# Kernel optimization log

Measured on AMD Instinct MI355X. Metric: run time of the kernel, lower is better.

## Reference

```python
import jax, jax.numpy as jnp
import numpy as np

D_IN = 512
D = 1024      # new_embed_dim
H = 16        # num_heads
HD = D // H   # head_dim


def setup_inputs() -> dict:
    key = jax.random.key(0)
    ks = jax.random.split(key, 16)
    g = lambda k, shape, fan: jax.random.normal(k, shape, jnp.float32) / np.sqrt(fan)
    return {
        "x1": jax.random.normal(ks[0], (16, 1, D_IN), jnp.float32),
        "x2": jax.random.normal(ks[1], (16, 4096, D_IN), jnp.float32),
        "x3": jax.random.normal(ks[2], (16, 4096, D_IN), jnp.float32),
        # embedding1 (for x1) and embedding2 (used for BOTH x2 and x3, per source)
        "We1": g(ks[3], (D_IN, D), D_IN), "be1": jnp.zeros((D,), jnp.float32),
        "We2": g(ks[4], (D_IN, D), D_IN), "be2": jnp.zeros((D,), jnp.float32),
        "Wq": g(ks[5], (D, D), D), "bq": jnp.zeros((D,), jnp.float32),
        "Wk": g(ks[6], (D, D), D), "bk": jnp.zeros((D,), jnp.float32),
        "Wv": g(ks[7], (D, D), D), "bv": jnp.zeros((D,), jnp.float32),
        "Wo": g(ks[8], (D, D), D), "bo": jnp.zeros((D,), jnp.float32),
    }


def reference(x1, x2, x3, We1, be1, We2, be2, Wq, bq, Wk, bk, Wv, bv, Wo, bo):
    B = x1.shape[0]
    # embeddings (x3 intentionally uses embedding2's weights, matching source)
    x1e = x1 @ We1 + be1                      # [B,1,D]
    x2e = x2 @ We2 + be2                      # [B,S,D]
    x3e = x3 @ We2 + be2                      # [B,S,D]
    q = (x1e @ Wq + bq).reshape(B, -1, H, HD).transpose(0, 2, 1, 3)  # [B,H,1,HD]
    k = (x2e @ Wk + bk).reshape(B, -1, H, HD).transpose(0, 2, 1, 3)  # [B,H,S,HD]
    v = (x3e @ Wv + bv).reshape(B, -1, H, HD).transpose(0, 2, 1, 3)  # [B,H,S,HD]
    scale = jnp.asarray(np.sqrt(HD), q.dtype)
    attn = jax.nn.softmax(jnp.einsum("bhqd,bhkd->bhqk", q, k) / scale, axis=-1)
    # dropout is identity at inference (keras training=False default)
    av = jnp.einsum("bhqk,bhkd->bhqd", attn, v)          # [B,H,1,HD]
    av = av.transpose(0, 2, 1, 3).reshape(B, -1, D)      # [B,1,D]
    out = av @ Wo + bo                                   # [B,1,D]
    return jnp.squeeze(out, axis=1)                      # [B,D]
```

## Files before the change

kernel.cpp:

```cpp
#include <hip/hip_runtime.h>


#define DIN 512
#define DD  1024
#define NH  16
#define HD  64
#define BB  16
#define SS  4096
#define NCH 64

__device__ __forceinline__ int wave_id() {
    return __builtin_amdgcn_readfirstlane((int)(threadIdx.x >> 6));
}

__device__ __forceinline__ void tile_transpose(const float* __restrict__ in,
                                               float* __restrict__ out,
                                               int R, int C, int rblk, int cblk) {
    __shared__ float tl[32][33];
    const int tx = threadIdx.x & 31, ty = threadIdx.x >> 5;
    const int c0 = cblk * 32, r0 = rblk * 32;
#pragma unroll
    for (int k = 0; k < 4; ++k)
        tl[ty + k * 8][tx] = in[(size_t)(r0 + ty + k * 8) * C + c0 + tx];
    __syncthreads();
#pragma unroll
    for (int k = 0; k < 4; ++k)
        out[(size_t)(c0 + ty + k * 8) * R + r0 + tx] = tl[tx][ty + k * 8];
}

__global__ __launch_bounds__(256) void k_prep(const float* __restrict__ We2,
                                              const float* __restrict__ Wk,
                                              const float* __restrict__ be1,
                                              const float* __restrict__ bq,
                                              const float* __restrict__ bv,
                                              const float* __restrict__ bo,
                                              float* __restrict__ We2t,
                                              float* __restrict__ WkT,
                                              float* __restrict__ x1e,
                                              float* __restrict__ qb,
                                              float* __restrict__ av,
                                              float* __restrict__ out) {
    const int bx = blockIdx.x;
    if (bx < 512) {
        tile_transpose(We2, We2t, DIN, DD, bx >> 5, bx & 31);
    } else if (bx < 1536) {
        const int lb = bx - 512;
        tile_transpose(Wk, WkT, DD, DD, lb >> 5, lb & 31);
    } else {
        const int b = bx - 1536;
#pragma unroll
        for (int k = 0; k < 4; ++k) {
            const int c = k * 256 + threadIdx.x;
            x1e[(size_t)b * DD + c] = be1[c];
            qb[(size_t)b * DD + c]  = bq[c];
            av[(size_t)b * DD + c]  = bv[c];
            out[(size_t)b * DD + c] = bo[c];
        }
    }
}

template <int K, int N, int KS, bool HASB>
__global__ __launch_bounds__(256) void k_bmv2(const float* __restrict__ in,
                                              const float* __restrict__ W,
                                              const float* __restrict__ bias,
                                              float* __restrict__ out) {
    const int l = threadIdx.x & 63;
    const int c = blockIdx.x * 64 + l;
    const int wv = wave_id();
    constexpr int KCH = K / KS;
    constexpr int SUB = KCH / 4;
    const float* inb = in + (size_t)blockIdx.y * 16 * K;
    float acc[16];
#pragma unroll
    for (int r = 0; r < 16; ++r) acc[r] = 0.f;
    const int i0 = blockIdx.z * KCH + wv * SUB;
#pragma unroll 4
    for (int i = i0; i < i0 + SUB; ++i) {
        const float wval = W[(size_t)i * N + c];
#pragma unroll
        for (int r = 0; r < 16; ++r) acc[r] += inb[(size_t)r * K + i] * wval;
    }
    __shared__ float red[4][16][64];
#pragma unroll
    for (int r = 0; r < 16; ++r) red[wv][r][l] = acc[r];
    __syncthreads();
#pragma unroll
    for (int k = 0; k < 4; ++k) {
        const int r = wv + k * 4;
        float v = red[0][r][l] + red[1][r][l] + red[2][r][l] + red[3][r][l];
        float* dst = out + ((size_t)blockIdx.y * 16 + r) * N + c;
        if (KS == 1) {
            if (HASB) v += bias[c];
            *dst = v;
        } else {
            atomicAdd(dst, v);
        }
    }
}

__global__ __launch_bounds__(256) void k_u2(const float* __restrict__ q,
                                            const float* __restrict__ WkT,
                                            float* __restrict__ u) {
    const int h = blockIdx.y;
    const int l = threadIdx.x & 63;
    const int c = blockIdx.x * 64 + l;
    const int wv = wave_id();
    float acc[16];
#pragma unroll
    for (int bb = 0; bb < 16; ++bb) acc[bb] = 0.f;
#pragma unroll 4
    for (int dk = 0; dk < 16; ++dk) {
        const int d = wv * 16 + dk;
        const float wval = WkT[(size_t)(h * HD + d) * DD + c];
#pragma unroll
        for (int bb = 0; bb < 16; ++bb)
            acc[bb] += q[(size_t)bb * DD + h * HD + d] * wval;
    }
    __shared__ float red[4][16][64];
#pragma unroll
    for (int bb = 0; bb < 16; ++bb) red[wv][bb][l] = acc[bb];
    __syncthreads();
#pragma unroll
    for (int k = 0; k < 4; ++k) {
        const int bb = wv + k * 4;
        float v = red[0][bb][l] + red[1][bb][l] + red[2][bb][l] + red[3][bb][l];
        u[((size_t)bb * NH + h) * DD + c] = v;
    }
}

__global__ __launch_bounds__(512, 8) void k_attn(const float* __restrict__ x2,
                                                 const float* __restrict__ x3,
                                                 const float* __restrict__ w,
                                                 float* __restrict__ gp,
                                                 float* __restrict__ mls) {
    __shared__ __align__(16) float4 tile[64 * 33];
    __shared__ __align__(16) float etab[64 * 20];

    const int b = blockIdx.y, ch = blockIdx.x;
    const int l = threadIdx.x & 63;
    const int wv = wave_id();
    const int h0 = wv * 2;
    const int s0 = ch * 64;
    const float4* wp = (const float4*)(w + ((size_t)b * NH + h0) * DIN);
    const float4* x2f = (const float4*)x2 + ((size_t)b * SS + s0) * (DIN / 4);

    const int srow = threadIdx.x >> 5;
    const int sc4  = threadIdx.x & 31;
    float4 r0 = x2f[(size_t)(srow)      * 128 + sc4];
    float4 r1 = x2f[(size_t)(srow + 16) * 128 + sc4];
    float4 r2 = x2f[(size_t)(srow + 32) * 128 + sc4];
    float4 r3 = x2f[(size_t)(srow + 48) * 128 + sc4];
    float a0 = 0.f, a1 = 0.f;
    for (int kt = 0; kt < 4; ++kt) {
        __syncthreads();
        tile[(srow)      * 33 + sc4] = r0;
        tile[(srow + 16) * 33 + sc4] = r1;
        tile[(srow + 32) * 33 + sc4] = r2;
        tile[(srow + 48) * 33 + sc4] = r3;
        __syncthreads();
        if (kt < 3) {
            const int kc = (kt + 1) * 32 + sc4;
            r0 = x2f[(size_t)(srow)      * 128 + kc];
            r1 = x2f[(size_t)(srow + 16) * 128 + kc];
            r2 = x2f[(size_t)(srow + 32) * 128 + kc];
            r3 = x2f[(size_t)(srow + 48) * 128 + kc];
        }
#pragma unroll 8
        for (int c4 = 0; c4 < 32; ++c4) {
            const float4 x = tile[l * 33 + c4];
            const float4 q0 = wp[kt * 32 + c4];
            const float4 q1 = wp[128 + kt * 32 + c4];
            a0 += x.x * q0.x + x.y * q0.y + x.z * q0.z + x.w * q0.w;
            a1 += x.x * q1.x + x.y * q1.y + x.z * q1.z + x.w * q1.w;
        }
    }

    const float sc0 = a0 * 0.125f, sc1 = a1 * 0.125f;
    float m0 = sc0, m1 = sc1;
#pragma unroll
    for (int off = 1; off < 64; off <<= 1) {
        m0 = fmaxf(m0, __shfl_xor(m0, off));
        m1 = fmaxf(m1, __shfl_xor(m1, off));
    }
    const float e0 = __expf(sc0 - m0), e1 = __expf(sc1 - m1);
    etab[l * 20 + h0]     = e0;
    etab[l * 20 + h0 + 1] = e1;
    float ls0 = e0, ls1 = e1;
#pragma unroll
    for (int off = 1; off < 64; off <<= 1) {
        ls0 += __shfl_xor(ls0, off);
        ls1 += __shfl_xor(ls1, off);
    }
    if (l == 0) {
        float* dst = mls + (((size_t)b * NCH + ch) * NH + h0) * 2;
        dst[0] = m0; dst[1] = ls0;
        dst[2] = m1; dst[3] = ls1;
    }
    __syncthreads();

    const int colh = wv & 1;
    const int h4 = (wv >> 1) * 4;
    const float4* x3f = (const float4*)(x3 + ((size_t)b * SS + s0) * DIN)
                        + colh * 64 + l;
    float4 A0 = make_float4(0.f, 0.f, 0.f, 0.f);
    float4 A1 = make_float4(0.f, 0.f, 0.f, 0.f);
    float4 A2 = make_float4(0.f, 0.f, 0.f, 0.f);
    float4 A3 = make_float4(0.f, 0.f, 0.f, 0.f);

    float4 p0 = x3f[0 * 128], p1 = x3f[1 * 128];
    float4 p2 = x3f[2 * 128], p3 = x3f[3 * 128];
#pragma unroll 4
    for (int j = 0; j < 64; ++j) {
        const float4 xv = p0;
        p0 = p1; p1 = p2; p2 = p3;
        const int jn = (j + 4 < 64) ? (j + 4) : 63;
        p3 = x3f[(size_t)jn * 128];
        const float4 e4 = *(const float4*)&etab[j * 20 + h4];
        A0.x += e4.x * xv.x; A0.y += e4.x * xv.y; A0.z += e4.x * xv.z; A0.w += e4.x * xv.w;
        A1.x += e4.y * xv.x; A1.y += e4.y * xv.y; A1.z += e4.y * xv.z; A1.w += e4.y * xv.w;
        A2.x += e4.z * xv.x; A2.y += e4.z * xv.y; A2.z += e4.z * xv.z; A2.w += e4.z * xv.w;
        A3.x += e4.w * xv.x; A3.y += e4.w * xv.y; A3.z += e4.w * xv.z; A3.w += e4.w * xv.w;
    }

    float* gb = gp + ((size_t)(b * NCH + ch) * NH + h4) * DIN + colh * 256 + 4 * l;
    *(float4*)(gb + 0 * DIN) = A0;
    *(float4*)(gb + 1 * DIN) = A1;
    *(float4*)(gb + 2 * DIN) = A2;
    *(float4*)(gb + 3 * DIN) = A3;
}

__global__ __launch_bounds__(256) void k_greduce2(const float* __restrict__ gp,
                                                  const float* __restrict__ mls,
                                                  float* __restrict__ g) {
    const int bx = blockIdx.x;
    const int pair = bx >> 1;
    const int b = pair >> 4, h = pair & 15;
    const int i = (bx & 1) * 256 + threadIdx.x;
    const float* mbase = mls + ((size_t)b * NCH * NH + h) * 2;
    float M = -1e30f;
#pragma unroll 8
    for (int ch = 0; ch < NCH; ++ch)
        M = fmaxf(M, mbase[(size_t)ch * NH * 2]);
    float L = 0.f;
#pragma unroll 8
    for (int ch = 0; ch < NCH; ++ch)
        L += __expf(mbase[(size_t)ch * NH * 2] - M) * mbase[(size_t)ch * NH * 2 + 1];
    const float invL = 1.f / L;
    const float* gpb = gp + ((size_t)(b * NCH) * NH + h) * DIN + i;
    float acc = 0.f;
#pragma unroll 8
    for (int ch = 0; ch < NCH; ++ch)
        acc += __expf(mbase[(size_t)ch * NH * 2] - M) * gpb[(size_t)ch * NH * DIN];
    g[(size_t)pair * DIN + i] = acc * invL;
}

__global__ __launch_bounds__(256) void k_av_at(const float* __restrict__ G2,
                                               const float* __restrict__ Wv,
                                               float* __restrict__ av) {
    const int h = blockIdx.x;
    const int l = threadIdx.x & 63;
    const int wv = wave_id();
    const int c0 = blockIdx.y * 128 + wv * 32;
    float acc[16];
#pragma unroll
    for (int bb = 0; bb < 16; ++bb) acc[bb] = 0.f;
#pragma unroll 4
    for (int c = c0; c < c0 + 32; ++c) {
        const float wval = Wv[(size_t)c * DD + h * HD + l];
#pragma unroll
        for (int bb = 0; bb < 16; ++bb)
            acc[bb] += G2[((size_t)bb * NH + h) * DD + c] * wval;
    }
    __shared__ float red[4][16][64];
#pragma unroll
    for (int bb = 0; bb < 16; ++bb) red[wv][bb][l] = acc[bb];
    __syncthreads();
#pragma unroll
    for (int k = 0; k < 4; ++k) {
        const int bb = wv + k * 4;
        float v = red[0][bb][l] + red[1][bb][l] + red[2][bb][l] + red[3][bb][l];
        atomicAdd(&av[(size_t)bb * DD + h * HD + l], v);
    }
}

extern "C" void kernel_launch(void* const* d_in, const int* in_sizes, int n_in,
                              void* d_out, int out_size, void* d_ws, size_t ws_size,
                              hipStream_t stream) {
    const float* x1  = (const float*)d_in[0];
    const float* x2  = (const float*)d_in[1];
    const float* x3  = (const float*)d_in[2];
    const float* We1 = (const float*)d_in[3];
    const float* be1 = (const float*)d_in[4];
    const float* We2 = (const float*)d_in[5];
    const float* be2 = (const float*)d_in[6];
    const float* Wq  = (const float*)d_in[7];
    const float* bq  = (const float*)d_in[8];
    const float* Wk  = (const float*)d_in[9];
    const float* bk  = (const float*)d_in[10];
    const float* Wv  = (const float*)d_in[11];
    const float* bv  = (const float*)d_in[12];
    const float* Wo  = (const float*)d_in[13];
    const float* bo  = (const float*)d_in[14];
    (void)bk;
    float* out = (float*)d_out;

    char* ws = (char*)d_ws;
    size_t off = 0;
    auto alloc = [&](size_t bytes) -> void* {
        void* p = ws + off;
        off = (off + bytes + 255) & ~(size_t)255;
        return p;
    };
    float* We2t = (float*)alloc((size_t)DD * DIN * 4);
    float* WkT  = (float*)alloc((size_t)DD * DD * 4);
    float* x1e  = (float*)alloc((size_t)BB * DD * 4);
    float* qb   = (float*)alloc((size_t)BB * DD * 4);
    float* u    = (float*)alloc((size_t)BB * NH * DD * 4);
    float* wv_  = (float*)alloc((size_t)BB * NH * DIN * 4);
    float* g    = (float*)alloc((size_t)BB * NH * DIN * 4);
    float* G2   = (float*)alloc((size_t)BB * NH * DD * 4);
    float* av   = (float*)alloc((size_t)BB * DD * 4);
    float* gp   = (float*)alloc((size_t)BB * NCH * NH * DIN * 4);
    float* mls  = (float*)alloc((size_t)BB * NCH * NH * 2 * 4);

    k_prep<<<1552, 256, 0, stream>>>(We2, Wk, be1, bq, bv, bo,
                                     We2t, WkT, x1e, qb, av, out);
    k_bmv2<DIN, DD, 8, false><<<dim3(DD / 64, 1, 8), 256, 0, stream>>>(x1, We1, nullptr, x1e);
    k_bmv2<DD, DD, 8, false><<<dim3(DD / 64, 1, 8), 256, 0, stream>>>(x1e, Wq, nullptr, qb);
    k_u2<<<dim3(DD / 64, NH), 256, 0, stream>>>(qb, WkT, u);
    k_bmv2<DD, DIN, 1, false><<<dim3(DIN / 64, BB * NH / 16, 1), 256, 0, stream>>>(u, We2t, nullptr, wv_);
    k_attn<<<dim3(NCH, BB), 512, 0, stream>>>(x2, x3, wv_, gp, mls);
    k_greduce2<<<BB * NH * 2, 256, 0, stream>>>(gp, mls, g);
    k_bmv2<DIN, DD, 1, true><<<dim3(DD / 64, BB * NH / 16, 1), 256, 0, stream>>>(g, We2, be2, G2);
    k_av_at<<<dim3(NH, 8), 256, 0, stream>>>(G2, Wv, av);
    k_bmv2<DD, DD, 8, false><<<dim3(DD / 64, 1, 8), 256, 0, stream>>>(av, Wo, nullptr, out);
}
```

Measured before the change: 446.0 us.

## Rebalance attention scoring to 4 heads per wave with split-K LDS reduction

The attention kernel's score phase now gives each wave 4 heads over half of the input dimension, and the two halves are combined through shared memory, so each LDS tile load serves more heads. The tile and exp-table buffers are aliased to cut shared memory use, and the x3 prefetch is issued before the barrier. The group-reduce kernel is vectorised with float4 and uses fewer, narrower blocks, and several matvec loops are unrolled by 8. The change adds barriers and a reduction step, and only half the waves do the softmax work.

```diff
diff --git a/kernel.cpp b/kernel.cpp
--- a/kernel.cpp
+++ b/kernel.cpp
@@ -74,7 +74,7 @@
 #pragma unroll
     for (int r = 0; r < 16; ++r) acc[r] = 0.f;
     const int i0 = blockIdx.z * KCH + wv * SUB;
-#pragma unroll 4
+#pragma unroll 8
     for (int i = i0; i < i0 + SUB; ++i) {
         const float wval = W[(size_t)i * N + c];
 #pragma unroll
@@ -108,7 +108,7 @@
     float acc[16];
 #pragma unroll
     for (int bb = 0; bb < 16; ++bb) acc[bb] = 0.f;
-#pragma unroll 4
+#pragma unroll 8
     for (int dk = 0; dk < 16; ++dk) {
         const int d = wv * 16 + dk;
         const float wval = WkT[(size_t)(h * HD + d) * DD + c];
@@ -133,13 +133,18 @@
                                                  const float* __restrict__ w,
                                                  float* __restrict__ gp,
                                                  float* __restrict__ mls) {
-    __shared__ __align__(16) float4 tile[64 * 33];
-    __shared__ __align__(16) float etab[64 * 20];
+    __shared__ __align__(16) char smem[64 * 33 * 16];
+    float4* tile = (float4*)smem;
+    float*  scp  = (float*)smem;
+    float*  etab = (float*)(smem + 8192);
 
     const int b = blockIdx.y, ch = blockIdx.x;
     const int l = threadIdx.x & 63;
     const int wv = wave_id();
-    const int h0 = wv * 2;
+    const int hq  = wv & 3;
+    const int ch2 = wv >> 2;
+    const int h0 = hq * 4;
+    const int c4b = ch2 * 16;
     const int s0 = ch * 64;
     const float4* wp = (const float4*)(w + ((size_t)b * NH + h0) * DIN);
     const float4* x2f = (const float4*)x2 + ((size_t)b * SS + s0) * (DIN / 4);
@@ -150,7 +155,7 @@
     float4 r1 = x2f[(size_t)(srow + 16) * 128 + sc4];
     float4 r2 = x2f[(size_t)(srow + 32) * 128 + sc4];
     float4 r3 = x2f[(size_t)(srow + 48) * 128 + sc4];
-    float a0 = 0.f, a1 = 0.f;
+    float a0 = 0.f, a1 = 0.f, a2 = 0.f, a3 = 0.f;
     for (int kt = 0; kt < 4; ++kt) {
         __syncthreads();
         tile[(srow)      * 33 + sc4] = r0;
@@ -166,49 +171,75 @@
             r3 = x2f[(size_t)(srow + 48) * 128 + kc];
         }
 #pragma unroll 8
-        for (int c4 = 0; c4 < 32; ++c4) {
-            const float4 x = tile[l * 33 + c4];
-            const float4 q0 = wp[kt * 32 + c4];
-            const float4 q1 = wp[128 + kt * 32 + c4];
+        for (int k = 0; k < 16; ++k) {
+            const float4 x = tile[l * 33 + c4b + k];
+            const float4 q0 = wp[      kt * 32 + c4b + k];
+            const float4 q1 = wp[128 + kt * 32 + c4b + k];
+            const float4 q2 = wp[256 + kt * 32 + c4b + k];
+            const float4 q3 = wp[384 + kt * 32 + c4b + k];
             a0 += x.x * q0.x + x.y * q0.y + x.z * q0.z + x.w * q0.w;
             a1 += x.x * q1.x + x.y * q1.y + x.z * q1.z + x.w * q1.w;
-        }
-    }
-
-    const float sc0 = a0 * 0.125f, sc1 = a1 * 0.125f;
-    float m0 = sc0, m1 = sc1;
-#pragma unroll
-    for (int off = 1; off < 64; off <<= 1) {
-        m0 = fmaxf(m0, __shfl_xor(m0, off));
-        m1 = fmaxf(m1, __shfl_xor(m1, off));
-    }
-    const float e0 = __expf(sc0 - m0), e1 = __expf(sc1 - m1);
-    etab[l * 20 + h0]     = e0;
-    etab[l * 20 + h0 + 1] = e1;
-    float ls0 = e0, ls1 = e1;
-#pragma unroll
-    for (int off = 1; off < 64; off <<= 1) {
-        ls0 += __shfl_xor(ls0, off);
-        ls1 += __shfl_xor(ls1, off);
-    }
-    if (l == 0) {
-        float* dst = mls + (((size_t)b * NCH + ch) * NH + h0) * 2;
-        dst[0] = m0; dst[1] = ls0;
-        dst[2] = m1; dst[3] = ls1;
-    }
-    __syncthreads();
+            a2 += x.x * q2.x + x.y * q2.y + x.z * q2.z + x.w * q2.w;
+            a3 += x.x * q3.x + x.y * q3.y + x.z * q3.z + x.w * q3.w;
+        }
+    }
+
+    __syncthreads();
+    if (ch2 == 1) {
+        scp[(hq * 4 + 0) * 64 + l] = a0;
+        scp[(hq * 4 + 1) * 64 + l] = a1;
+        scp[(hq * 4 + 2) * 64 + l] = a2;
+        scp[(hq * 4 + 3) * 64 + l] = a3;
+    }
+    __syncthreads();
+
+    if (ch2 == 0) {
+        a0 += scp[(hq * 4 + 0) * 64 + l];
+        a1 += scp[(hq * 4 + 1) * 64 + l];
+        a2 += scp[(hq * 4 + 2) * 64 + l];
+        a3 += scp[(hq * 4 + 3) * 64 + l];
+        const float sc0 = a0 * 0.125f, sc1 = a1 * 0.125f;
+        const float sc2 = a2 * 0.125f, sc3 = a3 * 0.125f;
+        float m0 = sc0, m1 = sc1, m2 = sc2, m3 = sc3;
+#pragma unroll
+        for (int off = 1; off < 64; off <<= 1) {
+            m0 = fmaxf(m0, __shfl_xor(m0, off));
+            m1 = fmaxf(m1, __shfl_xor(m1, off));
+            m2 = fmaxf(m2, __shfl_xor(m2, off));
+            m3 = fmaxf(m3, __shfl_xor(m3, off));
+        }
+        const float e0 = __expf(sc0 - m0), e1 = __expf(sc1 - m1);
+        const float e2 = __expf(sc2 - m2), e3 = __expf(sc3 - m3);
+        *(float4*)&etab[l * 20 + h0] = make_float4(e0, e1, e2, e3);
+        float ls0 = e0, ls1 = e1, ls2 = e2, ls3 = e3;
+#pragma unroll
+        for (int off = 1; off < 64; off <<= 1) {
+            ls0 += __shfl_xor(ls0, off);
+            ls1 += __shfl_xor(ls1, off);
+            ls2 += __shfl_xor(ls2, off);
+            ls3 += __shfl_xor(ls3, off);
+        }
+        if (l == 0) {
+            float* dst = mls + (((size_t)b * NCH + ch) * NH + h0) * 2;
+            dst[0] = m0; dst[1] = ls0;
+            dst[2] = m1; dst[3] = ls1;
+            dst[4] = m2; dst[5] = ls2;
+            dst[6] = m3; dst[7] = ls3;
+        }
+    }
 
     const int colh = wv & 1;
     const int h4 = (wv >> 1) * 4;
     const float4* x3f = (const float4*)(x3 + ((size_t)b * SS + s0) * DIN)
                         + colh * 64 + l;
+    float4 p0 = x3f[0 * 128], p1 = x3f[1 * 128];
+    float4 p2 = x3f[2 * 128], p3 = x3f[3 * 128];
+    __syncthreads();
+
     float4 A0 = make_float4(0.f, 0.f, 0.f, 0.f);
     float4 A1 = make_float4(0.f, 0.f, 0.f, 0.f);
     float4 A2 = make_float4(0.f, 0.f, 0.f, 0.f);
     float4 A3 = make_float4(0.f, 0.f, 0.f, 0.f);
-
-    float4 p0 = x3f[0 * 128], p1 = x3f[1 * 128];
-    float4 p2 = x3f[2 * 128], p3 = x3f[3 * 128];
 #pragma unroll 4
     for (int j = 0; j < 64; ++j) {
         const float4 xv = p0;
@@ -229,13 +260,12 @@
     *(float4*)(gb + 3 * DIN) = A3;
 }
 
-__global__ __launch_bounds__(256) void k_greduce2(const float* __restrict__ gp,
+__global__ __launch_bounds__(128) void k_greduce2(const float* __restrict__ gp,
                                                   const float* __restrict__ mls,
                                                   float* __restrict__ g) {
-    const int bx = blockIdx.x;
-    const int pair = bx >> 1;
+    const int pair = blockIdx.x;
     const int b = pair >> 4, h = pair & 15;
-    const int i = (bx & 1) * 256 + threadIdx.x;
+    const int t = threadIdx.x;
     const float* mbase = mls + ((size_t)b * NCH * NH + h) * 2;
     float M = -1e30f;
 #pragma unroll 8
@@ -246,12 +276,16 @@
     for (int ch = 0; ch < NCH; ++ch)
         L += __expf(mbase[(size_t)ch * NH * 2] - M) * mbase[(size_t)ch * NH * 2 + 1];
     const float invL = 1.f / L;
-    const float* gpb = gp + ((size_t)(b * NCH) * NH + h) * DIN + i;
-    float acc = 0.f;
-#pragma unroll 8
-    for (int ch = 0; ch < NCH; ++ch)
-        acc += __expf(mbase[(size_t)ch * NH * 2] - M) * gpb[(size_t)ch * NH * DIN];
-    g[(size_t)pair * DIN + i] = acc * invL;
+    const float4* gpb = (const float4*)(gp + ((size_t)(b * NCH) * NH + h) * DIN) + t;
+    float4 acc = make_float4(0.f, 0.f, 0.f, 0.f);
+#pragma unroll 8
+    for (int ch = 0; ch < NCH; ++ch) {
+        const float f = __expf(mbase[(size_t)ch * NH * 2] - M);
+        const float4 v = gpb[(size_t)ch * NH * (DIN / 4)];
+        acc.x += f * v.x; acc.y += f * v.y; acc.z += f * v.z; acc.w += f * v.w;
+    }
+    acc.x *= invL; acc.y *= invL; acc.z *= invL; acc.w *= invL;
+    ((float4*)(g + (size_t)pair * DIN))[t] = acc;
 }
 
 __global__ __launch_bounds__(256) void k_av_at(const float* __restrict__ G2,
@@ -264,7 +298,7 @@
     float acc[16];
 #pragma unroll
     for (int bb = 0; bb < 16; ++bb) acc[bb] = 0.f;
-#pragma unroll 4
+#pragma unroll 8
     for (int c = c0; c < c0 + 32; ++c) {
         const float wval = Wv[(size_t)c * DD + h * HD + l];
 #pragma unroll
@@ -330,7 +364,7 @@
     k_u2<<<dim3(DD / 64, NH), 256, 0, stream>>>(qb, WkT, u);
     k_bmv2<DD, DIN, 1, false><<<dim3(DIN / 64, BB * NH / 16, 1), 256, 0, stream>>>(u, We2t, nullptr, wv_);
     k_attn<<<dim3(NCH, BB), 512, 0, stream>>>(x2, x3, wv_, gp, mls);
-    k_greduce2<<<BB * NH * 2, 256, 0, stream>>>(gp, mls, g);
+    k_greduce2<<<BB * NH, 128, 0, stream>>>(gp, mls, g);
     k_bmv2<DIN, DD, 1, true><<<dim3(DD / 64, BB * NH / 16, 1), 256, 0, stream>>>(g, We2, be2, G2);
     k_av_at<<<dim3(NH, 8), 256, 0, stream>>>(G2, Wv, av);
     k_bmv2<DD, DD, 8, false><<<dim3(DD / 64, 1, 8), 256, 0, stream>>>(av, Wo, nullptr, out);
```

Result: slower. 466.0 us (+4.5%).

## Double attention chunk size, use nontemporal streaming loads, vectorize partial reduce

Applied to the files above, without the earlier changes.

Each attention block now covers 128 sequence rows instead of 64, which halves the number of chunks and the partial-output traffic. x2, x3 and the partials are read with nontemporal loads. The first x3 prefetch is moved before the barrier, the softmax-partial reduce is vectorized with float4, and several small GEMV loops get a higher unroll factor. The price is half as many attention blocks (512) on a large GPU, which may lower latency hiding, plus higher register and LDS use per block.

```diff
diff --git a/kernel.cpp b/kernel.cpp
--- a/kernel.cpp
+++ b/kernel.cpp
@@ -7,7 +7,14 @@
 #define HD  64
 #define BB  16
 #define SS  4096
-#define NCH 64
+#define NCH 32
+
+typedef float vf4 __attribute__((ext_vector_type(4)));
+
+__device__ __forceinline__ float4 ldnt(const float4* p) {
+    vf4 v = __builtin_nontemporal_load((const vf4*)p);
+    return make_float4(v[0], v[1], v[2], v[3]);
+}
 
 __device__ __forceinline__ int wave_id() {
     return __builtin_amdgcn_readfirstlane((int)(threadIdx.x >> 6));
@@ -74,7 +81,7 @@
 #pragma unroll
     for (int r = 0; r < 16; ++r) acc[r] = 0.f;
     const int i0 = blockIdx.z * KCH + wv * SUB;
-#pragma unroll 4
+#pragma unroll 8
     for (int i = i0; i < i0 + SUB; ++i) {
         const float wval = W[(size_t)i * N + c];
 #pragma unroll
@@ -108,7 +115,7 @@
     float acc[16];
 #pragma unroll
     for (int bb = 0; bb < 16; ++bb) acc[bb] = 0.f;
-#pragma unroll 4
+#pragma unroll 8
     for (int dk = 0; dk < 16; ++dk) {
         const int d = wv * 16 + dk;
         const float wval = WkT[(size_t)(h * HD + d) * DD + c];
@@ -134,23 +141,49 @@
                                                  float* __restrict__ gp,
                                                  float* __restrict__ mls) {
     __shared__ __align__(16) float4 tile[64 * 33];
-    __shared__ __align__(16) float etab[64 * 20];
+    __shared__ __align__(16) float etab[128 * 20];
 
     const int b = blockIdx.y, ch = blockIdx.x;
     const int l = threadIdx.x & 63;
     const int wv = wave_id();
     const int h0 = wv * 2;
-    const int s0 = ch * 64;
+    const int s0 = ch * 128;
     const float4* wp = (const float4*)(w + ((size_t)b * NH + h0) * DIN);
     const float4* x2f = (const float4*)x2 + ((size_t)b * SS + s0) * (DIN / 4);
 
     const int srow = threadIdx.x >> 5;
     const int sc4  = threadIdx.x & 31;
-    float4 r0 = x2f[(size_t)(srow)      * 128 + sc4];
-    float4 r1 = x2f[(size_t)(srow + 16) * 128 + sc4];
-    float4 r2 = x2f[(size_t)(srow + 32) * 128 + sc4];
-    float4 r3 = x2f[(size_t)(srow + 48) * 128 + sc4];
-    float a0 = 0.f, a1 = 0.f;
+    float4 r0 = ldnt(&x2f[(size_t)(srow)      * 128 + sc4]);
+    float4 r1 = ldnt(&x2f[(size_t)(srow + 16) * 128 + sc4]);
+    float4 r2 = ldnt(&x2f[(size_t)(srow + 32) * 128 + sc4]);
+    float4 r3 = ldnt(&x2f[(size_t)(srow + 48) * 128 + sc4]);
+    float a00 = 0.f, a10 = 0.f;
+    float a01 = 0.f, a11 = 0.f;
+
+    for (int kt = 0; kt < 4; ++kt) {
+        __syncthreads();
+        tile[(srow)      * 33 + sc4] = r0;
+        tile[(srow + 16) * 33 + sc4] = r1;
+        tile[(srow + 32) * 33 + sc4] = r2;
+        tile[(srow + 48) * 33 + sc4] = r3;
+        __syncthreads();
+        {
+            const int rb = (kt < 3) ? 0 : 64;
+            const int kc = ((kt < 3) ? (kt + 1) : 0) * 32 + sc4;
+            r0 = ldnt(&x2f[(size_t)(rb + srow)      * 128 + kc]);
+            r1 = ldnt(&x2f[(size_t)(rb + srow + 16) * 128 + kc]);
+            r2 = ldnt(&x2f[(size_t)(rb + srow + 32) * 128 + kc]);
+            r3 = ldnt(&x2f[(size_t)(rb + srow + 48) * 128 + kc]);
+        }
+#pragma unroll 8
+        for (int c4 = 0; c4 < 32; ++c4) {
+            const float4 x = tile[l * 33 + c4];
+            const float4 q0 = wp[kt * 32 + c4];
+            const float4 q1 = wp[128 + kt * 32 + c4];
+            a00 += x.x * q0.x + x.y * q0.y + x.z * q0.z + x.w * q0.w;
+            a10 += x.x * q1.x + x.y * q1.y + x.z * q1.z + x.w * q1.w;
+        }
+    }
     for (int kt = 0; kt < 4; ++kt) {
         __syncthreads();
         tile[(srow)      * 33 + sc4] = r0;
@@ -160,32 +193,36 @@
         __syncthreads();
         if (kt < 3) {
             const int kc = (kt + 1) * 32 + sc4;
-            r0 = x2f[(size_t)(srow)      * 128 + kc];
-            r1 = x2f[(size_t)(srow + 16) * 128 + kc];
-            r2 = x2f[(size_t)(srow + 32) * 128 + kc];
-            r3 = x2f[(size_t)(srow + 48) * 128 + kc];
+            r0 = ldnt(&x2f[(size_t)(64 + srow)      * 128 + kc]);
+            r1 = ldnt(&x2f[(size_t)(64 + srow + 16) * 128 + kc]);
+            r2 = ldnt(&x2f[(size_t)(64 + srow + 32) * 128 + kc]);
+            r3 = ldnt(&x2f[(size_t)(64 + srow + 48) * 128 + kc]);
         }
 #pragma unroll 8
         for (int c4 = 0; c4 < 32; ++c4) {
             const float4 x = tile[l * 33 + c4];
             const float4 q0 = wp[kt * 32 + c4];
             const float4 q1 = wp[128 + kt * 32 + c4];
-            a0 += x.x * q0.x + x.y * q0.y + x.z * q0.z + x.w * q0.w;
-            a1 += x.x * q1.x + x.y * q1.y + x.z * q1.z + x.w * q1.w;
-        }
-    }
-
-    const float sc0 = a0 * 0.125f, sc1 = a1 * 0.125f;
-    float m0 = sc0, m1 = sc1;
+            a01 += x.x * q0.x + x.y * q0.y + x.z * q0.z + x.w * q0.w;
+            a11 += x.x * q1.x + x.y * q1.y + x.z * q1.z + x.w * q1.w;
+        }
+    }
+
+    const float sc00 = a00 * 0.125f, sc10 = a10 * 0.125f;
+    const float sc01 = a01 * 0.125f, sc11 = a11 * 0.125f;
+    float m0 = fmaxf(sc00, sc01), m1 = fmaxf(sc10, sc11);
 #pragma unroll
     for (int off = 1; off < 64; off <<= 1) {
         m0 = fmaxf(m0, __shfl_xor(m0, off));
         m1 = fmaxf(m1, __shfl_xor(m1, off));
     }
-    const float e0 = __expf(sc0 - m0), e1 = __expf(sc1 - m1);
-    etab[l * 20 + h0]     = e0;
-    etab[l * 20 + h0 + 1] = e1;
-    float ls0 = e0, ls1 = e1;
+    const float e00 = __expf(sc00 - m0), e01 = __expf(sc01 - m0);
+    const float e10 = __expf(sc10 - m1), e11 = __expf(sc11 - m1);
+    etab[l * 20 + h0]            = e00;
+    etab[l * 20 + h0 + 1]        = e10;
+    etab[(64 + l) * 20 + h0]     = e01;
+    etab[(64 + l) * 20 + h0 + 1] = e11;
+    float ls0 = e00 + e01, ls1 = e10 + e11;
 #pragma unroll
     for (int off = 1; off < 64; off <<= 1) {
         ls0 += __shfl_xor(ls0, off);
@@ -196,25 +233,25 @@
         dst[0] = m0; dst[1] = ls0;
         dst[2] = m1; dst[3] = ls1;
     }
-    __syncthreads();
 
     const int colh = wv & 1;
     const int h4 = (wv >> 1) * 4;
     const float4* x3f = (const float4*)(x3 + ((size_t)b * SS + s0) * DIN)
                         + colh * 64 + l;
+    float4 p0 = ldnt(&x3f[0 * 128]), p1 = ldnt(&x3f[1 * 128]);
+    float4 p2 = ldnt(&x3f[2 * 128]), p3 = ldnt(&x3f[3 * 128]);
+    __syncthreads();
+
     float4 A0 = make_float4(0.f, 0.f, 0.f, 0.f);
     float4 A1 = make_float4(0.f, 0.f, 0.f, 0.f);
     float4 A2 = make_float4(0.f, 0.f, 0.f, 0.f);
     float4 A3 = make_float4(0.f, 0.f, 0.f, 0.f);
-
-    float4 p0 = x3f[0 * 128], p1 = x3f[1 * 128];
-    float4 p2 = x3f[2 * 128], p3 = x3f[3 * 128];
 #pragma unroll 4
-    for (int j = 0; j < 64; ++j) {
+    for (int j = 0; j < 128; ++j) {
         const float4 xv = p0;
         p0 = p1; p1 = p2; p2 = p3;
-        const int jn = (j + 4 < 64) ? (j + 4) : 63;
-        p3 = x3f[(size_t)jn * 128];
+        const int jn = (j + 4 < 128) ? (j + 4) : 127;
+        p3 = ldnt(&x3f[(size_t)jn * 128]);
         const float4 e4 = *(const float4*)&etab[j * 20 + h4];
         A0.x += e4.x * xv.x; A0.y += e4.x * xv.y; A0.z += e4.x * xv.z; A0.w += e4.x * xv.w;
         A1.x += e4.y * xv.x; A1.y += e4.y * xv.y; A1.z += e4.y * xv.z; A1.w += e4.y * xv.w;
@@ -229,13 +266,12 @@
     *(float4*)(gb + 3 * DIN) = A3;
 }
 
-__global__ __launch_bounds__(256) void k_greduce2(const float* __restrict__ gp,
+__global__ __launch_bounds__(128) void k_greduce2(const float* __restrict__ gp,
                                                   const float* __restrict__ mls,
                                                   float* __restrict__ g) {
-    const int bx = blockIdx.x;
-    const int pair = bx >> 1;
+    const int pair = blockIdx.x;
     const int b = pair >> 4, h = pair & 15;
-    const int i = (bx & 1) * 256 + threadIdx.x;
+    const int t = threadIdx.x;
     const float* mbase = mls + ((size_t)b * NCH * NH + h) * 2;
     float M = -1e30f;
 #pragma unroll 8
@@ -246,12 +282,16 @@
     for (int ch = 0; ch < NCH; ++ch)
         L += __expf(mbase[(size_t)ch * NH * 2] - M) * mbase[(size_t)ch * NH * 2 + 1];
     const float invL = 1.f / L;
-    const float* gpb = gp + ((size_t)(b * NCH) * NH + h) * DIN + i;
-    float acc = 0.f;
-#pragma unroll 8
-    for (int ch = 0; ch < NCH; ++ch)
-        acc += __expf(mbase[(size_t)ch * NH * 2] - M) * gpb[(size_t)ch * NH * DIN];
-    g[(size_t)pair * DIN + i] = acc * invL;
+    const float4* gpb = (const float4*)(gp + ((size_t)(b * NCH) * NH + h) * DIN) + t;
+    float4 acc = make_float4(0.f, 0.f, 0.f, 0.f);
+#pragma unroll 8
+    for (int ch = 0; ch < NCH; ++ch) {
+        const float f = __expf(mbase[(size_t)ch * NH * 2] - M);
+        const float4 v = ldnt(&gpb[(size_t)ch * NH * (DIN / 4)]);
+        acc.x += f * v.x; acc.y += f * v.y; acc.z += f * v.z; acc.w += f * v.w;
+    }
+    acc.x *= invL; acc.y *= invL; acc.z *= invL; acc.w *= invL;
+    ((float4*)(g + (size_t)pair * DIN))[t] = acc;
 }
 
 __global__ __launch_bounds__(256) void k_av_at(const float* __restrict__ G2,
@@ -264,7 +304,7 @@
     float acc[16];
 #pragma unroll
     for (int bb = 0; bb < 16; ++bb) acc[bb] = 0.f;
-#pragma unroll 4
+#pragma unroll 8
     for (int c = c0; c < c0 + 32; ++c) {
         const float wval = Wv[(size_t)c * DD + h * HD + l];
 #pragma unroll
@@ -330,7 +370,7 @@
     k_u2<<<dim3(DD / 64, NH), 256, 0, stream>>>(qb, WkT, u);
     k_bmv2<DD, DIN, 1, false><<<dim3(DIN / 64, BB * NH / 16, 1), 256, 0, stream>>>(u, We2t, nullptr, wv_);
     k_attn<<<dim3(NCH, BB), 512, 0, stream>>>(x2, x3, wv_, gp, mls);
-    k_greduce2<<<BB * NH * 2, 256, 0, stream>>>(gp, mls, g);
+    k_greduce2<<<BB * NH, 128, 0, stream>>>(gp, mls, g);
     k_bmv2<DIN, DD, 1, true><<<dim3(DD / 64, BB * NH / 16, 1), 256, 0, stream>>>(g, We2, be2, G2);
     k_av_at<<<dim3(NH, 8), 256, 0, stream>>>(G2, Wv, av);
     k_bmv2<DD, DD, 8, false><<<dim3(DD / 64, 1, 8), 256, 0, stream>>>(av, Wo, nullptr, out);
```

Measured after the change: 453.6 us. No clear change (+1.7%).
